# Kernel optimization log

Measured on AMD Instinct MI355X. Metric: run time of the kernel, lower is better.

Reference implementation:

```python
import jax, jax.numpy as jnp
import numpy as np

D = 16          # input_dim
H = 64          # hidden per tiny h-model
HG = 64 * D     # hidden of joint g model = 1024
B = 32768       # batch


def _init_linear(key, out_dim, in_dim):
    # torch nn.Linear default init: U(-1/sqrt(in), 1/sqrt(in)) for W and b
    kw, kb = jax.random.split(key)
    bound = 1.0 / np.sqrt(in_dim)
    W = jax.random.uniform(kw, (out_dim, in_dim), minval=-bound, maxval=bound, dtype=jnp.float32)
    b = jax.random.uniform(kb, (out_dim,), minval=-bound, maxval=bound, dtype=jnp.float32)
    return W, b


def setup_inputs() -> dict:
    key = jax.random.key(0)
    keys = jax.random.split(key, 16)
    x = jax.random.normal(keys[0], (B, 2 * D), dtype=jnp.float32)

    # Stacked weights for the D tiny h-models (1->64->64->64->64->1)
    def stack_h(k, out_dim, in_dim):
        ks = jax.random.split(k, D)
        Ws, bs = [], []
        for kk in ks:
            W, b = _init_linear(kk, out_dim, in_dim)
            Ws.append(W); bs.append(b)
        return jnp.stack(Ws), jnp.stack(bs)

    hW1, hb1 = stack_h(keys[1], H, 1)    # [D,64,1], [D,64]
    hW2, hb2 = stack_h(keys[2], H, H)    # [D,64,64]
    hW3, hb3 = stack_h(keys[3], H, H)
    hW4, hb4 = stack_h(keys[4], H, H)
    hW5, hb5 = stack_h(keys[5], 1, H)    # [D,1,64], [D,1]

    gW1, gb1 = _init_linear(keys[6], HG, D)
    gW2, gb2 = _init_linear(keys[7], HG, HG)
    gW3, gb3 = _init_linear(keys[8], HG, HG)
    gW4, gb4 = _init_linear(keys[9], HG, HG)
    gW5, gb5 = _init_linear(keys[10], 1, HG)

    return {
        "x": x,
        "hW1": hW1, "hb1": hb1, "hW2": hW2, "hb2": hb2,
        "hW3": hW3, "hb3": hb3, "hW4": hW4, "hb4": hb4,
        "hW5": hW5, "hb5": hb5,
        "gW1": gW1, "gb1": gb1, "gW2": gW2, "gb2": gb2,
        "gW3": gW3, "gb3": gb3, "gW4": gW4, "gb4": gb4,
        "gW5": gW5, "gb5": gb5,
    }


def reference(x, hW1, hb1, hW2, hb2, hW3, hb3, hW4, hb4, hW5, hb5,
              gW1, gb1, gW2, gb2, gW3, gb3, gW4, gb4, gW5, gb5):
    first_half = x[:, :D]    # [B, D] -> g branch
    second_half = x[:, D:]   # [B, D] -> D tiny h models, one scalar each

    # --- h branch: D independent 1->64->64->64->64->1 MLPs, batched ---
    # layer 1: scalar input per model; hW1[...,0] has shape [D, H]
    h = jax.nn.relu(second_half[:, :, None] * hW1[:, :, 0][None] + hb1[None])  # [B, D, H]
    h = jax.nn.relu(jnp.einsum('bdh,dgh->bdg', h, hW2) + hb2[None])            # [B, D, H]
    h = jax.nn.relu(jnp.einsum('bdh,dgh->bdg', h, hW3) + hb3[None])
    h = jax.nn.relu(jnp.einsum('bdh,dgh->bdg', h, hW4) + hb4[None])
    outputs_h = jnp.einsum('bdh,doh->bdo', h, hW5)[:, :, 0] + hb5[None, :, 0]  # [B, D]

    # --- g branch: D -> 64D -> ... -> 1 MLP ---
    g = jax.nn.relu(first_half @ gW1.T + gb1)  # [B, HG]
    g = jax.nn.relu(g @ gW2.T + gb2)
    g = jax.nn.relu(g @ gW3.T + gb3)
    g = jax.nn.relu(g @ gW4.T + gb4)
    outputs_g = g @ gW5.T + gb5                # [B, 1]

    return outputs_h, outputs_g
```

## Files before the change

kernel.cpp:

```cpp
#include <hip/hip_runtime.h>

#define B_ROWS 32768
#define D_NETS 16
#define MWH    1048576
#define GW1OFF (3 * MWH)
#define HPOFF  (GW1OFF + 16384)

typedef _Float16 half8 __attribute__((ext_vector_type(8)));
typedef _Float16 half4 __attribute__((ext_vector_type(4)));
typedef __attribute__((ext_vector_type(16))) float f32x16;

#define MFMA16 __builtin_amdgcn_mfma_f32_32x32x16_f16

__global__ void pack_f16(const float* __restrict__ gW1,
                         const float* __restrict__ gW2,
                         const float* __restrict__ gW3,
                         const float* __restrict__ gW4,
                         const float* __restrict__ hW2,
                         const float* __restrict__ hW3,
                         const float* __restrict__ hW4,
                         _Float16* __restrict__ ws) {
    const int p = blockIdx.x * 256 + threadIdx.x;
    const float* src;
    size_t dst;
    if (p < 393216) {
        const int lz = p >> 17;
        const int pl = p & 131071;
        const float* W = (lz == 0) ? gW2 : (lz == 1) ? gW3 : gW4;
        const int l = pl & 63, g = (pl >> 6) & 31, ks = pl >> 11;
        src = &W[(size_t)(g * 32 + (l & 31)) * 1024 + ks * 16 + (l >> 5) * 8];
        dst = (size_t)lz * MWH + (size_t)pl * 8;
    } else if (p < 395264) {
        const int q = p - 393216;
        const int l = q & 63, g = q >> 6;
        src = &gW1[(g * 32 + (l & 31)) * 16 + (l >> 5) * 8];
        dst = GW1OFF + (size_t)q * 8;
    } else {
        const int q = p - 395264;
        const int l = q & 63;
        const int sub = (q >> 6) & 7;
        const int ks = sub >> 1, g = sub & 1;
        const int dL = q >> 9;
        const int d = dL / 3, L = dL - d * 3;
        const float* W = (L == 0) ? hW2 : (L == 1) ? hW3 : hW4;
        src = &W[d * 4096 + (g * 32 + (l & 31)) * 64 + ks * 16 + (l >> 5) * 8];
        dst = HPOFF + (size_t)q * 8;
    }
    half8 v;
    #pragma unroll
    for (int kk = 0; kk < 8; ++kk) v[kk] = (_Float16)src[kk];
    *(half8*)&ws[dst] = v;
}

__global__ __launch_bounds__(256, 4) void h_net_mfma(
    const float* __restrict__ x,
    const float* __restrict__ hW1, const float* __restrict__ hb1,
    const float* __restrict__ hb2, const float* __restrict__ hb3,
    const float* __restrict__ hb4,
    const float* __restrict__ hW5, const float* __restrict__ hb5,
    const _Float16* __restrict__ ws,
    float* __restrict__ out)
{
    __shared__ _Float16 sA[8192];
    __shared__ float s_w1[64], s_b1[64], s_bs[3][64], s_w5[64];

    const int t = threadIdx.x;
    const int d = blockIdx.y;
    const int row0 = blockIdx.x * 128;
    const int l = t & 63, wv = t >> 6;
    const int l31 = l & 31, lk = l >> 5;

    if (t < 64) {
        s_w1[t]    = hW1[d * 64 + t];
        s_b1[t]    = hb1[d * 64 + t];
        s_bs[0][t] = hb2[d * 64 + t];
        s_bs[1][t] = hb3[d * 64 + t];
        s_bs[2][t] = hb4[d * 64 + t];
        s_w5[t]    = hW5[d * 64 + t];
    }
    __syncthreads();

    {
        const int row = t >> 1, jh = t & 1, rg = row >> 5, r31 = row & 31;
        const float sv = x[(size_t)(row0 + row) * 32 + 16 + d];
        #pragma unroll
        for (int jj = 0; jj < 32; ++jj) {
            const int j = jh * 32 + jj;
            const float a = fmaxf(fmaf(sv, s_w1[j], s_b1[j]), 0.f);
            const int ks = j >> 4;
            const int li = ((((j >> 3) & 1) << 5) | r31) ^ (ks << 3);
            sA[((rg * 4 + ks) * 64 + li) * 8 + (j & 7)] = (_Float16)a;
        }
    }
    __syncthreads();

    const _Float16* hp = ws + HPOFF + (size_t)d * 3 * 4096;

    #pragma unroll 1
    for (int L = 0; L < 3; ++L) {
        const _Float16* W = hp + (size_t)L * 4096;
        half8 B[4][2], A[4];
        #pragma unroll
        for (int ks = 0; ks < 4; ++ks) {
            B[ks][0] = *(const half8*)&W[((ks * 2 + 0) * 64 + l) * 8];
            B[ks][1] = *(const half8*)&W[((ks * 2 + 1) * 64 + l) * 8];
            A[ks] = *(const half8*)&sA[((wv * 4 + ks) * 64 + (l ^ (ks << 3))) * 8];
        }
        f32x16 acc[2];
        #pragma unroll
        for (int nt = 0; nt < 2; ++nt) {
            const float bv = s_bs[L][nt * 32 + l31];
            #pragma unroll
            for (int r = 0; r < 16; ++r) acc[nt][r] = bv;
        }
        #pragma unroll
        for (int ks = 0; ks < 4; ++ks) {
            acc[0] = MFMA16(A[ks], B[ks][0], acc[0], 0, 0, 0);
            acc[1] = MFMA16(A[ks], B[ks][1], acc[1], 0, 0, 0);
        }
        __syncthreads();
        #pragma unroll
        for (int nt = 0; nt < 2; ++nt) {
            #pragma unroll
            for (int r = 0; r < 16; ++r) {
                const int r31 = (r & 3) + 8 * (r >> 2) + 4 * lk;
                const int col = nt * 32 + l31;
                const float v = fmaxf(acc[nt][r], 0.f);
                const int ks = col >> 4;
                const int li = ((((col >> 3) & 1) << 5) | r31) ^ (ks << 3);
                sA[((wv * 4 + ks) * 64 + li) * 8 + (col & 7)] = (_Float16)v;
            }
        }
        __syncthreads();
    }

    {
        const int row = t >> 1, jh = t & 1, rg = row >> 5, r31 = row & 31;
        float s = 0.f;
        #pragma unroll
        for (int ks2 = 0; ks2 < 2; ++ks2) {
            const int ks = jh * 2 + ks2;
            #pragma unroll
            for (int h2 = 0; h2 < 2; ++h2) {
                const int li = ((h2 << 5) | r31) ^ (ks << 3);
                half8 v = *(const half8*)&sA[((rg * 4 + ks) * 64 + li) * 8];
                const float* w = &s_w5[ks * 16 + h2 * 8];
                #pragma unroll
                for (int kk = 0; kk < 8; ++kk)
                    s = fmaf((float)v[kk], w[kk], s);
            }
        }
        s += __shfl_xor(s, 1);
        if (jh == 0) out[(size_t)(row0 + row) * 16 + d] = s + hb5[d];
    }
}

__global__ __launch_bounds__(1024, 4) void g_fused_v6(
    const float* __restrict__ x,
    const _Float16* __restrict__ ws,
    const float* __restrict__ gb1, const float* __restrict__ gb2,
    const float* __restrict__ gb3, const float* __restrict__ gb4,
    const float* __restrict__ gW5, const float* __restrict__ gb5,
    float* __restrict__ out)
{
    __shared__ _Float16 sA[65536];
    __shared__ float s_w5f[1024];
    __shared__ float s_red[1024];
    __shared__ float s_bias[3][1024];

    const int t = threadIdx.x;
    const int l = t & 63, wv = t >> 6;
    const int l31 = l & 31, lk = l >> 5;
    const int n0 = wv * 64;
    const int row0 = blockIdx.x * 64;

    s_w5f[t] = gW5[t];
    s_bias[0][t] = gb2[t];
    s_bias[1][t] = gb3[t];
    s_bias[2][t] = gb4[t];

    f32x16 acc[2][2];

#define G_EPI()                                                              \
    {                                                                        \
        _Pragma("unroll")                                                    \
        for (int nt = 0; nt < 2; ++nt) {                                     \
            _Pragma("unroll")                                                \
            for (int rg = 0; rg < 2; ++rg) {                                 \
                _Pragma("unroll")                                            \
                for (int q = 0; q < 4; ++q) {                                \
                    half4 v;                                                 \
                    _Pragma("unroll")                                        \
                    for (int j = 0; j < 4; ++j)                              \
                        v[j] = (_Float16)fmaxf(acc[nt][rg][q * 4 + j], 0.f); \
                    const int ksn = wv * 4 + nt * 2 + (q >> 1);              \
                    const int li  = ((q & 1) << 5) | l31;                    \
                    *(half4*)&sA[((rg * 64 + ksn) * 64 + li) * 8 + lk * 4] = v; \
                }                                                            \
            }                                                                \
        }                                                                    \
    }

    {
        half8 xb[2];
        #pragma unroll
        for (int rg = 0; rg < 2; ++rg) {
            const float* xp = &x[(size_t)(row0 + rg * 32 + l31) * 32 + lk * 8];
            #pragma unroll
            for (int kk = 0; kk < 8; ++kk) xb[rg][kk] = (_Float16)xp[kk];
        }
        #pragma unroll
        for (int nt = 0; nt < 2; ++nt) {
            half8 wb = *(const half8*)&ws[GW1OFF + ((wv * 2 + nt) * 64 + l) * 8];
            #pragma unroll
            for (int rg = 0; rg < 2; ++rg) {
                #pragma unroll
                for (int r = 0; r < 16; ++r)
                    acc[nt][rg][r] =
                        gb1[n0 + nt * 32 + (r & 3) + 8 * (r >> 2) + 4 * lk];
                acc[nt][rg] = MFMA16(wb, xb[rg], acc[nt][rg], 0, 0, 0);
            }
        }
    }
    G_EPI();
    __syncthreads();

#define G_LA(ks, A_)                                                         \
    { A_[0] = *(const half8*)&sA[((ks) * 64 + l) * 8];                       \
      A_[1] = *(const half8*)&sA[((64 + (ks)) * 64 + l) * 8]; }
#define G_LB(ks, B_)                                                         \
    { const int _o = (ks) * 16384 + wv * 1024 + l * 8;                       \
      B_[0] = *(const half8*)&W[_o];                                         \
      B_[1] = *(const half8*)&W[_o + 512]; }
#define G_MM(A_, B_)                                                         \
    { __builtin_amdgcn_s_setprio(1);                                         \
      acc[0][0] = MFMA16(B_[0], A_[0], acc[0][0], 0, 0, 0);                  \
      acc[0][1] = MFMA16(B_[0], A_[1], acc[0][1], 0, 0, 0);                  \
      acc[1][0] = MFMA16(B_[1], A_[0], acc[1][0], 0, 0, 0);                  \
      acc[1][1] = MFMA16(B_[1], A_[1], acc[1][1], 0, 0, 0);                  \
      __builtin_amdgcn_s_setprio(0); }

    #pragma unroll 1
    for (int L = 0; L < 3; ++L) {
        const _Float16* W = ws + (size_t)L * MWH;

        half8 A0[2], A1[2], B0[2], B1[2];
        G_LA(0, A0); G_LB(0, B0);
        G_LA(1, A1); G_LB(1, B1);

        #pragma unroll
        for (int nt = 0; nt < 2; ++nt)
            #pragma unroll
            for (int rg = 0; rg < 2; ++rg)
                #pragma unroll
                for (int r = 0; r < 16; ++r)
                    acc[nt][rg][r] =
                        s_bias[L][n0 + nt * 32 + (r & 3) + 8 * (r >> 2) + 4 * lk];

        #pragma unroll 1
        for (int ks = 0; ks < 64; ks += 2) {
            G_MM(A0, B0);
            if (ks + 2 < 64) { G_LA(ks + 2, A0); G_LB(ks + 2, B0); }
            G_MM(A1, B1);
            if (ks + 3 < 64) { G_LA(ks + 3, A1); G_LB(ks + 3, B1); }
        }

        __syncthreads();
        G_EPI();
        __syncthreads();
    }
#undef G_LA
#undef G_LB
#undef G_MM
#undef G_EPI

    {
        const int row = t & 63;
        const int rg5 = row >> 5, r31 = row & 31;
        const int c = t >> 6;
        float s = 0.f;
        #pragma unroll
        for (int q = 0; q < 4; ++q) {
            #pragma unroll
            for (int kh = 0; kh < 2; ++kh) {
                half8 v = *(const half8*)&sA[((rg5 * 64 + c * 4 + q) * 64 +
                                             ((kh << 5) | r31)) * 8];
                const float* w = &s_w5f[(c * 4 + q) * 16 + kh * 8];
                #pragma unroll
                for (int kk = 0; kk < 8; ++kk)
                    s = fmaf((float)v[kk], w[kk], s);
            }
        }
        s_red[t] = s;
    }
    __syncthreads();
    if (t < 64) {
        float s = gb5[0];
        #pragma unroll
        for (int c = 0; c < 16; ++c) s += s_red[c * 64 + t];
        out[(size_t)B_ROWS * D_NETS + row0 + t] = s;
    }
}

extern "C" void kernel_launch(void* const* d_in, const int* in_sizes, int n_in,
                              void* d_out, int out_size, void* d_ws, size_t ws_size,
                              hipStream_t stream) {
    (void)in_sizes; (void)n_in; (void)out_size; (void)ws_size;

    const float* x   = (const float*)d_in[0];
    const float* hW1 = (const float*)d_in[1];
    const float* hb1 = (const float*)d_in[2];
    const float* hW2 = (const float*)d_in[3];
    const float* hb2 = (const float*)d_in[4];
    const float* hW3 = (const float*)d_in[5];
    const float* hb3 = (const float*)d_in[6];
    const float* hW4 = (const float*)d_in[7];
    const float* hb4 = (const float*)d_in[8];
    const float* hW5 = (const float*)d_in[9];
    const float* hb5 = (const float*)d_in[10];
    const float* gW1 = (const float*)d_in[11];
    const float* gb1 = (const float*)d_in[12];
    const float* gW2 = (const float*)d_in[13];
    const float* gb2 = (const float*)d_in[14];
    const float* gW3 = (const float*)d_in[15];
    const float* gb3 = (const float*)d_in[16];
    const float* gW4 = (const float*)d_in[17];
    const float* gb4 = (const float*)d_in[18];
    const float* gW5 = (const float*)d_in[19];
    const float* gb5 = (const float*)d_in[20];
    float* out = (float*)d_out;
    _Float16* wsh = (_Float16*)d_ws;

    pack_f16<<<1640, 256, 0, stream>>>(gW1, gW2, gW3, gW4, hW2, hW3, hW4, wsh);

    dim3 gh(B_ROWS / 128, D_NETS);
    h_net_mfma<<<gh, 256, 0, stream>>>(x, hW1, hb1, hb2, hb3, hb4,
                                       hW5, hb5, wsh, out);

    g_fused_v6<<<B_ROWS / 64, 1024, 0, stream>>>(x, wsh, gb1, gb2, gb3, gb4,
                                                 gW5, gb5, out);
}
```

Baseline: 265.0 us.

## Fuse tiny h-network MLPs into the g kernel tail, one wave per net

Removes the separate h_net_mfma launch and computes the 16 tiny h-MLPs at the end of the g kernel. Each of the 16 waves handles one h-net for the block's 64 rows, using its own 4096-half slice of the now-free shared buffer. Weights and biases are read straight from global memory instead of being staged in shared memory. This saves one kernel launch and its prologue. The cost is a serial tail appended to a heavy kernel and a reuse of the `acc` registers declared earlier in that kernel.

```diff
diff --git a/kernel.cpp b/kernel.cpp
--- a/kernel.cpp
+++ b/kernel.cpp
@@ -52,115 +52,16 @@
     *(half8*)&ws[dst] = v;
 }
 
-__global__ __launch_bounds__(256, 4) void h_net_mfma(
-    const float* __restrict__ x,
-    const float* __restrict__ hW1, const float* __restrict__ hb1,
-    const float* __restrict__ hb2, const float* __restrict__ hb3,
-    const float* __restrict__ hb4,
-    const float* __restrict__ hW5, const float* __restrict__ hb5,
-    const _Float16* __restrict__ ws,
-    float* __restrict__ out)
-{
-    __shared__ _Float16 sA[8192];
-    __shared__ float s_w1[64], s_b1[64], s_bs[3][64], s_w5[64];
-
-    const int t = threadIdx.x;
-    const int d = blockIdx.y;
-    const int row0 = blockIdx.x * 128;
-    const int l = t & 63, wv = t >> 6;
-    const int l31 = l & 31, lk = l >> 5;
-
-    if (t < 64) {
-        s_w1[t]    = hW1[d * 64 + t];
-        s_b1[t]    = hb1[d * 64 + t];
-        s_bs[0][t] = hb2[d * 64 + t];
-        s_bs[1][t] = hb3[d * 64 + t];
-        s_bs[2][t] = hb4[d * 64 + t];
-        s_w5[t]    = hW5[d * 64 + t];
-    }
-    __syncthreads();
-
-    {
-        const int row = t >> 1, jh = t & 1, rg = row >> 5, r31 = row & 31;
-        const float sv = x[(size_t)(row0 + row) * 32 + 16 + d];
-        #pragma unroll
-        for (int jj = 0; jj < 32; ++jj) {
-            const int j = jh * 32 + jj;
-            const float a = fmaxf(fmaf(sv, s_w1[j], s_b1[j]), 0.f);
-            const int ks = j >> 4;
-            const int li = ((((j >> 3) & 1) << 5) | r31) ^ (ks << 3);
-            sA[((rg * 4 + ks) * 64 + li) * 8 + (j & 7)] = (_Float16)a;
-        }
-    }
-    __syncthreads();
-
-    const _Float16* hp = ws + HPOFF + (size_t)d * 3 * 4096;
-
-    #pragma unroll 1
-    for (int L = 0; L < 3; ++L) {
-        const _Float16* W = hp + (size_t)L * 4096;
-        half8 B[4][2], A[4];
-        #pragma unroll
-        for (int ks = 0; ks < 4; ++ks) {
-            B[ks][0] = *(const half8*)&W[((ks * 2 + 0) * 64 + l) * 8];
-            B[ks][1] = *(const half8*)&W[((ks * 2 + 1) * 64 + l) * 8];
-            A[ks] = *(const half8*)&sA[((wv * 4 + ks) * 64 + (l ^ (ks << 3))) * 8];
-        }
-        f32x16 acc[2];
-        #pragma unroll
-        for (int nt = 0; nt < 2; ++nt) {
-            const float bv = s_bs[L][nt * 32 + l31];
-            #pragma unroll
-            for (int r = 0; r < 16; ++r) acc[nt][r] = bv;
-        }
-        #pragma unroll
-        for (int ks = 0; ks < 4; ++ks) {
-            acc[0] = MFMA16(A[ks], B[ks][0], acc[0], 0, 0, 0);
-            acc[1] = MFMA16(A[ks], B[ks][1], acc[1], 0, 0, 0);
-        }
-        __syncthreads();
-        #pragma unroll
-        for (int nt = 0; nt < 2; ++nt) {
-            #pragma unroll
-            for (int r = 0; r < 16; ++r) {
-                const int r31 = (r & 3) + 8 * (r >> 2) + 4 * lk;
-                const int col = nt * 32 + l31;
-                const float v = fmaxf(acc[nt][r], 0.f);
-                const int ks = col >> 4;
-                const int li = ((((col >> 3) & 1) << 5) | r31) ^ (ks << 3);
-                sA[((wv * 4 + ks) * 64 + li) * 8 + (col & 7)] = (_Float16)v;
-            }
-        }
-        __syncthreads();
-    }
-
-    {
-        const int row = t >> 1, jh = t & 1, rg = row >> 5, r31 = row & 31;
-        float s = 0.f;
-        #pragma unroll
-        for (int ks2 = 0; ks2 < 2; ++ks2) {
-            const int ks = jh * 2 + ks2;
-            #pragma unroll
-            for (int h2 = 0; h2 < 2; ++h2) {
-                const int li = ((h2 << 5) | r31) ^ (ks << 3);
-                half8 v = *(const half8*)&sA[((rg * 4 + ks) * 64 + li) * 8];
-                const float* w = &s_w5[ks * 16 + h2 * 8];
-                #pragma unroll
-                for (int kk = 0; kk < 8; ++kk)
-                    s = fmaf((float)v[kk], w[kk], s);
-            }
-        }
-        s += __shfl_xor(s, 1);
-        if (jh == 0) out[(size_t)(row0 + row) * 16 + d] = s + hb5[d];
-    }
-}
-
-__global__ __launch_bounds__(1024, 4) void g_fused_v6(
+__global__ __launch_bounds__(1024, 4) void g_fused_v7(
     const float* __restrict__ x,
     const _Float16* __restrict__ ws,
     const float* __restrict__ gb1, const float* __restrict__ gb2,
     const float* __restrict__ gb3, const float* __restrict__ gb4,
     const float* __restrict__ gW5, const float* __restrict__ gb5,
+    const float* __restrict__ hW1, const float* __restrict__ hb1,
+    const float* __restrict__ hb2, const float* __restrict__ hb3,
+    const float* __restrict__ hb4,
+    const float* __restrict__ hW5, const float* __restrict__ hb5,
     float* __restrict__ out)
 {
     __shared__ _Float16 sA[65536];
@@ -299,6 +200,91 @@
         #pragma unroll
         for (int c = 0; c < 16; ++c) s += s_red[c * 64 + t];
         out[(size_t)B_ROWS * D_NETS + row0 + t] = s;
+    }
+
+    {
+        _Float16* sN = &sA[wv * 4096];
+        const _Float16* hp = ws + HPOFF + (size_t)wv * 3 * 4096;
+        const int rgl = l >> 5;
+
+        {
+            const float x2 = x[(size_t)(row0 + l) * 32 + 16 + wv];
+            const float* w1 = &hW1[wv * 64];
+            const float* b1 = &hb1[wv * 64];
+            #pragma unroll
+            for (int ks = 0; ks < 4; ++ks) {
+                #pragma unroll
+                for (int kh = 0; kh < 2; ++kh) {
+                    half8 v;
+                    #pragma unroll
+                    for (int kk = 0; kk < 8; ++kk) {
+                        const int j = ks * 16 + kh * 8 + kk;
+                        v[kk] = (_Float16)fmaxf(fmaf(x2, w1[j], b1[j]), 0.f);
+                    }
+                    *(half8*)&sN[((rgl * 4 + ks) * 64 + ((kh << 5) | l31)) * 8] = v;
+                }
+            }
+        }
+
+        #pragma unroll 1
+        for (int L = 0; L < 3; ++L) {
+            const _Float16* W = hp + (size_t)L * 4096;
+            const float* hbL = ((L == 0) ? hb2 : (L == 1) ? hb3 : hb4) + wv * 64;
+
+            #pragma unroll
+            for (int ng = 0; ng < 2; ++ng)
+                #pragma unroll
+                for (int rg = 0; rg < 2; ++rg)
+                    #pragma unroll
+                    for (int r = 0; r < 16; ++r)
+                        acc[ng][rg][r] =
+                            hbL[ng * 32 + (r & 3) + 8 * (r >> 2) + 4 * lk];
+
+            #pragma unroll
+            for (int ks = 0; ks < 4; ++ks) {
+                half8 w0 = *(const half8*)&W[((ks * 2 + 0) * 64 + l) * 8];
+                half8 w1_ = *(const half8*)&W[((ks * 2 + 1) * 64 + l) * 8];
+                half8 a0 = *(const half8*)&sN[((0 * 4 + ks) * 64 + l) * 8];
+                half8 a1 = *(const half8*)&sN[((1 * 4 + ks) * 64 + l) * 8];
+                acc[0][0] = MFMA16(w0, a0, acc[0][0], 0, 0, 0);
+                acc[0][1] = MFMA16(w0, a1, acc[0][1], 0, 0, 0);
+                acc[1][0] = MFMA16(w1_, a0, acc[1][0], 0, 0, 0);
+                acc[1][1] = MFMA16(w1_, a1, acc[1][1], 0, 0, 0);
+            }
+
+            #pragma unroll
+            for (int ng = 0; ng < 2; ++ng)
+                #pragma unroll
+                for (int rg = 0; rg < 2; ++rg)
+                    #pragma unroll
+                    for (int q = 0; q < 4; ++q) {
+                        half4 v;
+                        #pragma unroll
+                        for (int j = 0; j < 4; ++j)
+                            v[j] = (_Float16)fmaxf(acc[ng][rg][q * 4 + j], 0.f);
+                        const int ksn = ng * 2 + (q >> 1);
+                        const int li  = ((q & 1) << 5) | l31;
+                        *(half4*)&sN[((rg * 4 + ksn) * 64 + li) * 8 + lk * 4] = v;
+                    }
+        }
+
+        {
+            const float* w5 = &hW5[wv * 64];
+            float s = 0.f;
+            #pragma unroll
+            for (int ks = 0; ks < 4; ++ks) {
+                #pragma unroll
+                for (int kh = 0; kh < 2; ++kh) {
+                    half8 v = *(const half8*)&sN[((rgl * 4 + ks) * 64 +
+                                                 ((kh << 5) | l31)) * 8];
+                    const float* w = &w5[ks * 16 + kh * 8];
+                    #pragma unroll
+                    for (int kk = 0; kk < 8; ++kk)
+                        s = fmaf((float)v[kk], w[kk], s);
+                }
+            }
+            out[(size_t)(row0 + l) * 16 + wv] = s + hb5[wv];
+        }
     }
 }
 
@@ -333,10 +319,7 @@
 
     pack_f16<<<1640, 256, 0, stream>>>(gW1, gW2, gW3, gW4, hW2, hW3, hW4, wsh);
 
-    dim3 gh(B_ROWS / 128, D_NETS);
-    h_net_mfma<<<gh, 256, 0, stream>>>(x, hW1, hb1, hb2, hb3, hb4,
-                                       hW5, hb5, wsh, out);
-
-    g_fused_v6<<<B_ROWS / 64, 1024, 0, stream>>>(x, wsh, gb1, gb2, gb3, gb4,
-                                                 gW5, gb5, out);
+    g_fused_v7<<<B_ROWS / 64, 1024, 0, stream>>>(
+        x, wsh, gb1, gb2, gb3, gb4, gW5, gb5,
+        hW1, hb1, hb2, hb3, hb4, hW5, hb5, out);
 }
```

New measurement: 251.8 us. -5.0%, faster.
